# Performance work log

Hardware: AMD Instinct MI355X
Metric: run time of the kernel (lower is better)

The kernel has to match this reference:

```python
import jax, jax.numpy as jnp
import numpy as np

B, N, C = 2, 3072, 768
H = 12                      # num_heads
HD = C // H                 # 64
D = HD // 2                 # 32, rope dim per axis
GRID_H, GRID_W = 48, 64     # 768/16, 1024/16 ; GRID_H*GRID_W == N
BASE = 100.0
EPS = 1e-5


def _rope_tables():
    # positions per token (row-major cartesian product of y,x)
    pos_y = np.repeat(np.arange(GRID_H), GRID_W)   # [N]
    pos_x = np.tile(np.arange(GRID_W), GRID_H)     # [N]
    seq_len = max(GRID_H, GRID_W)
    inv_freq = 1.0 / BASE ** (np.arange(0, D, 2, dtype=np.float32) / D)  # [D/2]
    t = np.arange(seq_len, dtype=np.float32)
    freqs = np.einsum('i,j->ij', t, inv_freq)            # [S, D/2]
    emb = np.concatenate([freqs, freqs], axis=-1)        # [S, D]
    cos, sin = np.cos(emb), np.sin(emb)
    # gather per-token, add head broadcast dims -> [1, 1, N, D]
    mk = lambda tbl, idx: jnp.asarray(tbl[idx][None, None], dtype=jnp.float32)
    return mk(cos, pos_x), mk(sin, pos_x), mk(cos, pos_y), mk(sin, pos_y)


def setup_inputs() -> dict:
    key = jax.random.key(0)
    ks = jax.random.split(key, 12)
    s = 0.02
    cos_x, sin_x, cos_y, sin_y = _rope_tables()
    return {
        'x': jax.random.normal(ks[0], (B, N, C), jnp.float32),
        'w_qkv': jax.random.normal(ks[1], (3 * C, C), jnp.float32) * s,
        'w_proj': jax.random.normal(ks[2], (C, C), jnp.float32) * s,
        'b_proj': jnp.zeros((C,), jnp.float32),
        'g1': jnp.ones((C,), jnp.float32),
        'beta1': jnp.zeros((C,), jnp.float32),
        'g2': jnp.ones((C,), jnp.float32),
        'beta2': jnp.zeros((C,), jnp.float32),
        'w_fc1': jax.random.normal(ks[3], (4 * C, C), jnp.float32) * s,
        'b_fc1': jnp.zeros((4 * C,), jnp.float32),
        'w_fc2': jax.random.normal(ks[4], (C, 4 * C), jnp.float32) * s,
        'b_fc2': jnp.zeros((C,), jnp.float32),
        'cos_x': cos_x, 'sin_x': sin_x, 'cos_y': cos_y, 'sin_y': sin_y,
    }


def _layernorm(x, g, b):
    m = x.mean(-1, keepdims=True)
    v = ((x - m) ** 2).mean(-1, keepdims=True)
    return (x - m) * jax.lax.rsqrt(v + EPS) * g + b


def _rope1d(tok, cos, sin):
    t1, t2 = jnp.split(tok, 2, axis=-1)
    rot = jnp.concatenate([-t2, t1], axis=-1)
    return tok * cos + rot * sin


def _rope2d(tok, cos_x, sin_x, cos_y, sin_y):
    # tok: [B, H, N, HD]; first half of HD is y-coords, second half x-coords
    ty, tx = jnp.split(tok, 2, axis=-1)
    return jnp.concatenate([_rope1d(ty, cos_y, sin_y), _rope1d(tx, cos_x, sin_x)], axis=-1)


def reference(x, w_qkv, w_proj, b_proj, g1, beta1, g2, beta2,
              w_fc1, b_fc1, w_fc2, b_fc2, cos_x, sin_x, cos_y, sin_y):
    # --- attention branch ---
    xn = _layernorm(x, g1, beta1)
    qkv = jnp.einsum('bnc,dc->bnd', xn, w_qkv)           # [B, N, 3C]
    qkv = qkv.reshape(B, N, 3, H, HD).transpose(0, 3, 2, 1, 4)  # [B, H, 3, N, HD]
    q, k, v = qkv[:, :, 0], qkv[:, :, 1], qkv[:, :, 2]
    q = _rope2d(q, cos_x, sin_x, cos_y, sin_y)
    k = _rope2d(k, cos_x, sin_x, cos_y, sin_y)
    scale = HD ** -0.5
    attn = jnp.einsum('bhqd,bhkd->bhqk', q, k) * scale   # [B, H, N, N]
    attn = jax.nn.softmax(attn, axis=-1)
    o = jnp.einsum('bhqk,bhkd->bhqd', attn, v)           # [B, H, N, HD]
    o = o.transpose(0, 2, 1, 3).reshape(B, N, C)
    o = jnp.einsum('bnc,dc->bnd', o, w_proj) + b_proj
    x = x + o
    # --- mlp branch ---
    xn = _layernorm(x, g2, beta2)
    h = jnp.einsum('bnc,hc->bnh', xn, w_fc1) + b_fc1
    h = jax.nn.gelu(h, approximate=False)                # torch nn.GELU default (erf)
    h = jnp.einsum('bnh,ch->bnc', h, w_fc2) + b_fc2
    return x + h
```

## Files before the change

kernel.cpp:

```cpp
#include <hip/hip_runtime.h>
#include <hip/hip_bf16.h>


#define Nn 3072
#define Cc 768
#define Hh 12
#define Mm 6144

typedef unsigned short ushort_t;
typedef unsigned int u32;
using s8v = __attribute__((ext_vector_type(8))) short;
using f4v = __attribute__((ext_vector_type(4))) float;

__device__ __forceinline__ ushort_t f2b(float x){
  u32 u = __float_as_uint(x);
  return (ushort_t)((u + 0x7fffu + ((u >> 16) & 1u)) >> 16);
}
__device__ __forceinline__ u32 pack2(float a, float b){
  return (u32)f2b(a) | ((u32)f2b(b) << 16);
}
__device__ __forceinline__ u32 pack2t(float a, float b){
  return (__float_as_uint(a) >> 16) | (__float_as_uint(b) & 0xffff0000u);
}
__device__ __forceinline__ float b2f(ushort_t u){
  return __uint_as_float(((u32)u) << 16);
}

#define GLD16(g, l) __builtin_amdgcn_global_load_lds( \
    (const __attribute__((address_space(1))) u32*)(g), \
    (__attribute__((address_space(3))) u32*)(l), 16, 0, 0)

__global__ __launch_bounds__(256) void cvt4_kernel(
    const float* __restrict__ a, ushort_t* __restrict__ oa, int na,
    const float* __restrict__ b, ushort_t* __restrict__ ob, int nb,
    const float* __restrict__ c, ushort_t* __restrict__ oc, int nc,
    const float* __restrict__ d, ushort_t* __restrict__ od)
{
  int i = (blockIdx.x*256 + threadIdx.x)*4;
  const float* src; ushort_t* dst;
  if (i < na)           { src = a + i;            dst = oa + i; }
  else if (i < na+nb)   { src = b + (i-na);       dst = ob + (i-na); }
  else if (i < na+nb+nc){ src = c + (i-na-nb);    dst = oc + (i-na-nb); }
  else                  { src = d + (i-na-nb-nc); dst = od + (i-na-nb-nc); }
  float4 v = *(const float4*)src;
  uint2 p; p.x = pack2(v.x, v.y); p.y = pack2(v.z, v.w);
  *(uint2*)dst = p;
}

__global__ __launch_bounds__(256) void ln_kernel(const float* __restrict__ in,
    const float* __restrict__ g, const float* __restrict__ be, ushort_t* __restrict__ out)
{
  int row = blockIdx.x;
  int tid = threadIdx.x;
  size_t base = (size_t)row * Cc;
  float v[3];
  #pragma unroll
  for (int i = 0; i < 3; ++i) v[i] = in[base + tid + i*256];
  __shared__ float red[8];
  float s = v[0]+v[1]+v[2];
  #pragma unroll
  for (int off=32; off; off>>=1) s += __shfl_xor(s, off);
  int wid = tid >> 6, lane = tid & 63;
  if (lane==0) red[wid] = s;
  __syncthreads();
  float mean = (red[0]+red[1]+red[2]+red[3]) * (1.f/Cc);
  float d = 0.f;
  #pragma unroll
  for (int i=0;i<3;++i){ float t = v[i]-mean; d += t*t; }
  #pragma unroll
  for (int off=32; off; off>>=1) d += __shfl_xor(d, off);
  if (lane==0) red[4+wid] = d;
  __syncthreads();
  float var  = (red[4]+red[5]+red[6]+red[7]) * (1.f/Cc);
  float rstd = rsqrtf(var + 1e-5f);
  #pragma unroll
  for (int i=0;i<3;++i){
    int idx = tid + i*256;
    out[base+idx] = f2b((v[i]-mean)*rstd*g[idx] + be[idx]);
  }
}

template<int EPI>
__global__ __launch_bounds__(256) void mgemm_kernel(
    const ushort_t* __restrict__ A, const ushort_t* __restrict__ W,
    const float* __restrict__ bias, const float* __restrict__ residf,
    void* __restrict__ outv, int Nd, int K)
{
  __shared__ __align__(16) ushort_t As[128*32];
  __shared__ __align__(16) ushort_t Ws[128*32];
  int tid = threadIdx.x;
  int w = tid >> 6, lane = tid & 63;
  int g = lane >> 4, c = lane & 15;
  int wr = w >> 1, wc = w & 1;
  int m0 = blockIdx.y * 128, n0 = blockIdx.x * 128;
  int srow = w*32 + (lane >> 2);
  int schunk = (lane & 3) * 8;
  const ushort_t* Ag = A + (size_t)(m0 + srow)*K + schunk;
  const ushort_t* Wg = W + (size_t)(n0 + srow)*K + schunk;
  ushort_t* Asl = &As[w*1024];
  ushort_t* Wsl = &Ws[w*1024];
  f4v acc[4][4] = {};
  for (int k0 = 0; k0 < K; k0 += 32) {
    __syncthreads();
    GLD16(Ag + k0,        Asl);
    GLD16(Ag + 16*K + k0, Asl + 512);
    GLD16(Wg + k0,        Wsl);
    GLD16(Wg + 16*K + k0, Wsl + 512);
    __syncthreads();
    s8v af[4], wf[4];
    #pragma unroll
    for (int i=0;i<4;++i) af[i] = *(const s8v*)&As[(wr*64 + i*16 + c)*32 + g*8];
    #pragma unroll
    for (int j=0;j<4;++j) wf[j] = *(const s8v*)&Ws[(wc*64 + j*16 + c)*32 + g*8];
    #pragma unroll
    for (int i=0;i<4;++i)
      #pragma unroll
      for (int j=0;j<4;++j)
        acc[i][j] = __builtin_amdgcn_mfma_f32_16x16x32_bf16(af[i], wf[j], acc[i][j], 0,0,0);
  }
  #pragma unroll
  for (int j=0;j<4;++j){
    int col = n0 + wc*64 + j*16 + c;
    float bv = (EPI != 0) ? bias[col] : 0.f;
    #pragma unroll
    for (int i=0;i<4;++i){
      int row0 = m0 + wr*64 + i*16 + g*4;
      #pragma unroll
      for (int r=0;r<4;++r){
        float v = acc[i][j][r];
        size_t off = (size_t)(row0 + r)*Nd + col;
        if (EPI == 0) {
          ((ushort_t*)outv)[off] = f2b(v);
        } else if (EPI == 2) {
          float t = v + bv;
          ((ushort_t*)outv)[off] = f2b(0.5f*t*(1.0f + erff(t*0.70710678118654752f)));
        } else {
          ((float*)outv)[off] = v + bv + residf[off];
        }
      }
    }
  }
}

__global__ __launch_bounds__(256) void repack_kernel(
    const ushort_t* __restrict__ qkv,
    const float* __restrict__ cx, const float* __restrict__ sx,
    const float* __restrict__ cy, const float* __restrict__ sy,
    ushort_t* __restrict__ Qb, ushort_t* __restrict__ Kb, ushort_t* __restrict__ Vt)
{
  __shared__ float Vls[64*68];
  int bh = blockIdx.y;
  int b = bh / Hh, h = bh - b*Hh;
  int n0 = blockIdx.x * 64;
  int tid = threadIdx.x;
  int tt = tid >> 2, cch = tid & 3;
  int n = n0 + tt;
  size_t rowbase = (size_t)(b*Nn + n) * 2304 + h*64;

  int half = cch >> 1, ibase = (cch & 1) * 8;
  int d1 = half*32 + ibase;
  const float* ct  = half ? cx : cy;
  const float* st_ = half ? sx : sy;
  float c1[8], s1[8], c2[8], s2[8];
  #pragma unroll
  for (int j=0;j<8;++j){
    c1[j] = ct[n*32 + ibase + j];       s1[j] = st_[n*32 + ibase + j];
    c2[j] = ct[n*32 + ibase + 16 + j];  s2[j] = st_[n*32 + ibase + 16 + j];
  }
  #pragma unroll
  for (int qk = 0; qk < 2; ++qk){
    const ushort_t* src = qkv + rowbase + qk*768;
    uint4 uv1 = *(const uint4*)(src + d1);
    uint4 uv2 = *(const uint4*)(src + d1 + 16);
    float v1[8], v2[8];
    v1[0]=b2f(uv1.x&0xffff); v1[1]=b2f(uv1.x>>16); v1[2]=b2f(uv1.y&0xffff); v1[3]=b2f(uv1.y>>16);
    v1[4]=b2f(uv1.z&0xffff); v1[5]=b2f(uv1.z>>16); v1[6]=b2f(uv1.w&0xffff); v1[7]=b2f(uv1.w>>16);
    v2[0]=b2f(uv2.x&0xffff); v2[1]=b2f(uv2.x>>16); v2[2]=b2f(uv2.y&0xffff); v2[3]=b2f(uv2.y>>16);
    v2[4]=b2f(uv2.z&0xffff); v2[5]=b2f(uv2.z>>16); v2[6]=b2f(uv2.w&0xffff); v2[7]=b2f(uv2.w>>16);
    float sc = qk ? 1.0f : 0.125f;
    float o1[8], o2[8];
    #pragma unroll
    for (int j=0;j<8;++j){
      o1[j] = (v1[j]*c1[j] - v2[j]*s1[j]) * sc;
      o2[j] = (v2[j]*c2[j] + v1[j]*s2[j]) * sc;
    }
    ushort_t* dst = (qk ? Kb : Qb) + ((size_t)bh*Nn + n)*64;
    uint4 u1, u2;
    u1.x = pack2(o1[0],o1[1]); u1.y = pack2(o1[2],o1[3]);
    u1.z = pack2(o1[4],o1[5]); u1.w = pack2(o1[6],o1[7]);
    u2.x = pack2(o2[0],o2[1]); u2.y = pack2(o2[2],o2[3]);
    u2.z = pack2(o2[4],o2[5]); u2.w = pack2(o2[6],o2[7]);
    *(uint4*)(dst + d1)      = u1;
    *(uint4*)(dst + d1 + 16) = u2;
  }

  {
    const ushort_t* src = qkv + rowbase + 1536 + cch*16;
    uint4 ua = *(const uint4*)(src);
    uint4 ub = *(const uint4*)(src + 8);
    float* lp = &Vls[tt*68 + cch*16];
    lp[0]=b2f(ua.x&0xffff); lp[1]=b2f(ua.x>>16); lp[2]=b2f(ua.y&0xffff); lp[3]=b2f(ua.y>>16);
    lp[4]=b2f(ua.z&0xffff); lp[5]=b2f(ua.z>>16); lp[6]=b2f(ua.w&0xffff); lp[7]=b2f(ua.w>>16);
    lp[8]=b2f(ub.x&0xffff); lp[9]=b2f(ub.x>>16); lp[10]=b2f(ub.y&0xffff); lp[11]=b2f(ub.y>>16);
    lp[12]=b2f(ub.z&0xffff); lp[13]=b2f(ub.z>>16); lp[14]=b2f(ub.w&0xffff); lp[15]=b2f(ub.w>>16);
  }
  __syncthreads();
  {
    int d = tid & 63, quarter = tid >> 6;
    float v[16];
    #pragma unroll
    for (int j=0;j<16;++j) v[j] = Vls[(quarter*16 + j)*68 + d];
    uint4 w0, w1;
    w0.x = pack2(v[0],v[1]);   w0.y = pack2(v[2],v[3]);
    w0.z = pack2(v[4],v[5]);   w0.w = pack2(v[6],v[7]);
    w1.x = pack2(v[8],v[9]);   w1.y = pack2(v[10],v[11]);
    w1.z = pack2(v[12],v[13]); w1.w = pack2(v[14],v[15]);
    ushort_t* dst = Vt + ((size_t)bh*64 + d)*Nn + n0 + quarter*16;
    *(uint4*)(dst)     = w0;
    *(uint4*)(dst + 8) = w1;
  }
}

__global__ __launch_bounds__(256) void fattn_kernel(
    const ushort_t* __restrict__ Qb, const ushort_t* __restrict__ Kb,
    const ushort_t* __restrict__ Vt, ushort_t* __restrict__ ob)
{
  __shared__ ushort_t Ks[64*72];
  __shared__ ushort_t Vts[64*72];
  __shared__ ushort_t Ps[4*32*72];
  int bh = blockIdx.y;
  int q0 = blockIdx.x * 128;
  int tid = threadIdx.x;
  int w = tid >> 6, lane = tid & 63, g = lane >> 4, c = lane & 15;

  const ushort_t* qpA = Qb + ((size_t)bh*Nn + q0 + w*32 + c)*64;
  const ushort_t* qpB = qpA + 16*64;
  s8v qA0 = *(const s8v*)(qpA + g*8);
  s8v qA1 = *(const s8v*)(qpA + 32 + g*8);
  s8v qB0 = *(const s8v*)(qpB + g*8);
  s8v qB1 = *(const s8v*)(qpB + 32 + g*8);

  s8v ones8;
  #pragma unroll
  for (int j=0;j<8;++j) ones8[j] = (short)0x3f80;

  f4v oA[4] = {}, oB[4] = {}, lA = {0,0,0,0}, lB = {0,0,0,0};
  const ushort_t* kbase = Kb + (size_t)bh*Nn*64;
  const ushort_t* vbase = Vt + (size_t)bh*64*Nn;
  ushort_t* pwA = &Ps[w*32*72];
  ushort_t* pwB = pwA + 16*72;

  int srow = tid >> 2;
  int scb  = (tid & 3) * 16;

  for (int kt = 0; kt < Nn/64; ++kt){
    __syncthreads();
    {
      const ushort_t* ksrc = kbase + (size_t)(kt*64 + srow)*64 + scb;
      *(uint4*)&Ks[srow*72 + scb]     = *(const uint4*)(ksrc);
      *(uint4*)&Ks[srow*72 + scb + 8] = *(const uint4*)(ksrc + 8);
      const ushort_t* vsrc = vbase + (size_t)srow*Nn + kt*64 + scb;
      *(uint4*)&Vts[srow*72 + scb]     = *(const uint4*)(vsrc);
      *(uint4*)&Vts[srow*72 + scb + 8] = *(const uint4*)(vsrc + 8);
    }
    __syncthreads();

    f4v sA[4], sB[4];
    #pragma unroll
    for (int t=0;t<4;++t){
      s8v ka  = *(const s8v*)&Ks[(t*16+c)*72 + g*8];
      s8v kb2 = *(const s8v*)&Ks[(t*16+c)*72 + 32 + g*8];
      f4v z = {0,0,0,0};
      z = __builtin_amdgcn_mfma_f32_16x16x32_bf16(ka,  qA0, z, 0,0,0);
      sA[t] = __builtin_amdgcn_mfma_f32_16x16x32_bf16(kb2, qA1, z, 0,0,0);
      f4v z2 = {0,0,0,0};
      z2 = __builtin_amdgcn_mfma_f32_16x16x32_bf16(ka,  qB0, z2, 0,0,0);
      sB[t] = __builtin_amdgcn_mfma_f32_16x16x32_bf16(kb2, qB1, z2, 0,0,0);
    }
    #pragma unroll
    for (int t=0;t<4;++t){
      uint2 pk;
      pk.x = pack2t(__expf(sA[t][0]), __expf(sA[t][1]));
      pk.y = pack2t(__expf(sA[t][2]), __expf(sA[t][3]));
      *(uint2*)&pwA[c*72 + t*16 + g*4] = pk;
      pk.x = pack2t(__expf(sB[t][0]), __expf(sB[t][1]));
      pk.y = pack2t(__expf(sB[t][2]), __expf(sB[t][3]));
      *(uint2*)&pwB[c*72 + t*16 + g*4] = pk;
    }
    asm volatile("s_waitcnt lgkmcnt(0)" ::: "memory");
    s8v pA0 = *(const s8v*)&pwA[c*72 + g*8];
    s8v pA1 = *(const s8v*)&pwA[c*72 + 32 + g*8];
    s8v pB0 = *(const s8v*)&pwB[c*72 + g*8];
    s8v pB1 = *(const s8v*)&pwB[c*72 + 32 + g*8];

    #pragma unroll
    for (int d=0;d<4;++d){
      s8v va = *(const s8v*)&Vts[(d*16+c)*72 + g*8];
      s8v vb = *(const s8v*)&Vts[(d*16+c)*72 + 32 + g*8];
      oA[d] = __builtin_amdgcn_mfma_f32_16x16x32_bf16(va, pA0, oA[d], 0,0,0);
      oA[d] = __builtin_amdgcn_mfma_f32_16x16x32_bf16(vb, pA1, oA[d], 0,0,0);
      oB[d] = __builtin_amdgcn_mfma_f32_16x16x32_bf16(va, pB0, oB[d], 0,0,0);
      oB[d] = __builtin_amdgcn_mfma_f32_16x16x32_bf16(vb, pB1, oB[d], 0,0,0);
    }
    lA = __builtin_amdgcn_mfma_f32_16x16x32_bf16(ones8, pA0, lA, 0,0,0);
    lA = __builtin_amdgcn_mfma_f32_16x16x32_bf16(ones8, pA1, lA, 0,0,0);
    lB = __builtin_amdgcn_mfma_f32_16x16x32_bf16(ones8, pB0, lB, 0,0,0);
    lB = __builtin_amdgcn_mfma_f32_16x16x32_bf16(ones8, pB1, lB, 0,0,0);
  }

  int b = bh / Hh, h = bh - b*Hh;
  {
    float rl = 1.0f / lA[0];
    size_t tok = (size_t)b*Nn + q0 + w*32 + c;
    ushort_t* op = ob + tok*768 + h*64;
    #pragma unroll
    for (int d=0;d<4;++d){
      uint2 pk;
      pk.x = pack2(oA[d][0]*rl, oA[d][1]*rl);
      pk.y = pack2(oA[d][2]*rl, oA[d][3]*rl);
      *(uint2*)&op[d*16 + g*4] = pk;
    }
  }
  {
    float rl = 1.0f / lB[0];
    size_t tok = (size_t)b*Nn + q0 + w*32 + 16 + c;
    ushort_t* op = ob + tok*768 + h*64;
    #pragma unroll
    for (int d=0;d<4;++d){
      uint2 pk;
      pk.x = pack2(oB[d][0]*rl, oB[d][1]*rl);
      pk.y = pack2(oB[d][2]*rl, oB[d][3]*rl);
      *(uint2*)&op[d*16 + g*4] = pk;
    }
  }
}

extern "C" void kernel_launch(void* const* d_in, const int* in_sizes, int n_in,
                              void* d_out, int out_size, void* d_ws, size_t ws_size,
                              hipStream_t stream)
{
  const float* x      = (const float*)d_in[0];
  const float* w_qkv  = (const float*)d_in[1];
  const float* w_proj = (const float*)d_in[2];
  const float* b_proj = (const float*)d_in[3];
  const float* g1     = (const float*)d_in[4];
  const float* be1    = (const float*)d_in[5];
  const float* g2     = (const float*)d_in[6];
  const float* be2    = (const float*)d_in[7];
  const float* w_fc1  = (const float*)d_in[8];
  const float* b_fc1  = (const float*)d_in[9];
  const float* w_fc2  = (const float*)d_in[10];
  const float* b_fc2  = (const float*)d_in[11];
  const float* cx     = (const float*)d_in[12];
  const float* sx     = (const float*)d_in[13];
  const float* cy     = (const float*)d_in[14];
  const float* sy     = (const float*)d_in[15];
  float* out = (float*)d_out;

  char* ws = (char*)d_ws;
  ushort_t* xnb   = (ushort_t*)(ws);
  ushort_t* Qb    = (ushort_t*)(ws + 9437184);
  ushort_t* Kb    = (ushort_t*)(ws + 18874368);
  float*    x1    = (float*)   (ws + 9437184);
  ushort_t* Vt    = (ushort_t*)(ws + 28311552);
  ushort_t* obb   = (ushort_t*)(ws + 37748736);
  ushort_t* qkvb  = (ushort_t*)(ws + 47185920);
  ushort_t* hb    = (ushort_t*)(ws + 47185920);
  ushort_t* wqkvb = (ushort_t*)(ws + 84934656);
  ushort_t* wprojb= (ushort_t*)(ws + 88473600);
  ushort_t* wfc1b = (ushort_t*)(ws + 89653248);
  ushort_t* wfc2b = (ushort_t*)(ws + 94371840);

  cvt4_kernel<<<(7077888/4)/256, 256, 0, stream>>>(
      w_qkv, wqkvb, 2304*768, w_proj, wprojb, 768*768,
      w_fc1, wfc1b, 3072*768, w_fc2, wfc2b);

  ln_kernel<<<Mm, 256, 0, stream>>>(x, g1, be1, xnb);
  mgemm_kernel<0><<<dim3(2304/128, Mm/128), 256, 0, stream>>>(xnb, wqkvb, nullptr, nullptr, qkvb, 2304, 768);
  repack_kernel<<<dim3(48, 24), 256, 0, stream>>>(qkvb, cx, sx, cy, sy, Qb, Kb, Vt);
  fattn_kernel<<<dim3(24, 24), 256, 0, stream>>>(Qb, Kb, Vt, obb);
  mgemm_kernel<1><<<dim3(768/128, Mm/128), 256, 0, stream>>>(obb, wprojb, b_proj, x, x1, 768, 768);
  ln_kernel<<<Mm, 256, 0, stream>>>(x1, g2, be2, xnb);
  mgemm_kernel<2><<<dim3(3072/128, Mm/128), 256, 0, stream>>>(xnb, wfc1b, b_fc1, nullptr, hb, 3072, 768);
  mgemm_kernel<1><<<dim3(768/128, Mm/128), 256, 0, stream>>>(hb, wfc2b, b_fc2, x1, out, 768, 3072);
}
```

Before: 468.0 us.

## Split attention keys across waves and narrow GEMM tiles for N=768 projections

The attention kernel now processes 64 queries per block, and each of the four waves handles a disjoint quarter of the keys. Waves load K and V fragments straight from global memory instead of staging them through shared LDS with block barriers. Partial outputs and row sums are combined through LDS at the end, and the grid doubles to 48x24 blocks. The projection and fc2 GEMMs get a 64-wide N tile so they launch more blocks, at the cost of less reuse per tile and a bf16 rounding of the partial attention outputs before the reduction.

```diff
diff --git a/kernel.cpp b/kernel.cpp
--- a/kernel.cpp
+++ b/kernel.cpp
@@ -80,47 +80,49 @@
   }
 }
 
-template<int EPI>
+template<int EPI, int NT>
 __global__ __launch_bounds__(256) void mgemm_kernel(
     const ushort_t* __restrict__ A, const ushort_t* __restrict__ W,
     const float* __restrict__ bias, const float* __restrict__ residf,
     void* __restrict__ outv, int Nd, int K)
 {
+  constexpr int JT = NT/32;
   __shared__ __align__(16) ushort_t As[128*32];
-  __shared__ __align__(16) ushort_t Ws[128*32];
+  __shared__ __align__(16) ushort_t Ws[NT*32];
   int tid = threadIdx.x;
   int w = tid >> 6, lane = tid & 63;
   int g = lane >> 4, c = lane & 15;
   int wr = w >> 1, wc = w & 1;
-  int m0 = blockIdx.y * 128, n0 = blockIdx.x * 128;
-  int srow = w*32 + (lane >> 2);
+  int m0 = blockIdx.y * 128, n0 = blockIdx.x * NT;
   int schunk = (lane & 3) * 8;
-  const ushort_t* Ag = A + (size_t)(m0 + srow)*K + schunk;
-  const ushort_t* Wg = W + (size_t)(n0 + srow)*K + schunk;
+  const ushort_t* Ag = A + (size_t)(m0 + w*32 + (lane >> 2))*K + schunk;
+  const ushort_t* Wg;
+  if constexpr (NT == 128) Wg = W + (size_t)(n0 + w*32 + (lane >> 2))*K + schunk;
+  else                     Wg = W + (size_t)(n0 + w*16 + (lane >> 2))*K + schunk;
   ushort_t* Asl = &As[w*1024];
-  ushort_t* Wsl = &Ws[w*1024];
-  f4v acc[4][4] = {};
+  ushort_t* Wsl = (NT == 128) ? &Ws[w*1024] : &Ws[w*512];
+  f4v acc[4][JT] = {};
   for (int k0 = 0; k0 < K; k0 += 32) {
     __syncthreads();
     GLD16(Ag + k0,        Asl);
     GLD16(Ag + 16*K + k0, Asl + 512);
     GLD16(Wg + k0,        Wsl);
-    GLD16(Wg + 16*K + k0, Wsl + 512);
+    if constexpr (NT == 128) GLD16(Wg + 16*K + k0, Wsl + 512);
     __syncthreads();
-    s8v af[4], wf[4];
+    s8v af[4], wf[JT];
     #pragma unroll
     for (int i=0;i<4;++i) af[i] = *(const s8v*)&As[(wr*64 + i*16 + c)*32 + g*8];
     #pragma unroll
-    for (int j=0;j<4;++j) wf[j] = *(const s8v*)&Ws[(wc*64 + j*16 + c)*32 + g*8];
+    for (int j=0;j<JT;++j) wf[j] = *(const s8v*)&Ws[(wc*(NT/2) + j*16 + c)*32 + g*8];
     #pragma unroll
     for (int i=0;i<4;++i)
       #pragma unroll
-      for (int j=0;j<4;++j)
+      for (int j=0;j<JT;++j)
         acc[i][j] = __builtin_amdgcn_mfma_f32_16x16x32_bf16(af[i], wf[j], acc[i][j], 0,0,0);
   }
   #pragma unroll
-  for (int j=0;j<4;++j){
-    int col = n0 + wc*64 + j*16 + c;
+  for (int j=0;j<JT;++j){
+    int col = n0 + wc*(NT/2) + j*16 + c;
     float bv = (EPI != 0) ? bias[col] : 0.f;
     #pragma unroll
     for (int i=0;i<4;++i){
@@ -221,118 +223,117 @@
   }
 }
 
-__global__ __launch_bounds__(256) void fattn_kernel(
+__global__ __launch_bounds__(256, 2) void fattn_kernel(
     const ushort_t* __restrict__ Qb, const ushort_t* __restrict__ Kb,
     const ushort_t* __restrict__ Vt, ushort_t* __restrict__ ob)
 {
-  __shared__ ushort_t Ks[64*72];
-  __shared__ ushort_t Vts[64*72];
-  __shared__ ushort_t Ps[4*32*72];
+  __shared__ __align__(16) char smem[36864];
+  __shared__ float Lred[256];
   int bh = blockIdx.y;
-  int q0 = blockIdx.x * 128;
+  int q0 = blockIdx.x * 64;
   int tid = threadIdx.x;
   int w = tid >> 6, lane = tid & 63, g = lane >> 4, c = lane & 15;
 
-  const ushort_t* qpA = Qb + ((size_t)bh*Nn + q0 + w*32 + c)*64;
-  const ushort_t* qpB = qpA + 16*64;
-  s8v qA0 = *(const s8v*)(qpA + g*8);
-  s8v qA1 = *(const s8v*)(qpA + 32 + g*8);
-  s8v qB0 = *(const s8v*)(qpB + g*8);
-  s8v qB1 = *(const s8v*)(qpB + 32 + g*8);
-
-  s8v ones8;
-  #pragma unroll
-  for (int j=0;j<8;++j) ones8[j] = (short)0x3f80;
-
-  f4v oA[4] = {}, oB[4] = {}, lA = {0,0,0,0}, lB = {0,0,0,0};
   const ushort_t* kbase = Kb + (size_t)bh*Nn*64;
   const ushort_t* vbase = Vt + (size_t)bh*64*Nn;
-  ushort_t* pwA = &Ps[w*32*72];
-  ushort_t* pwB = pwA + 16*72;
-
-  int srow = tid >> 2;
-  int scb  = (tid & 3) * 16;
-
-  for (int kt = 0; kt < Nn/64; ++kt){
-    __syncthreads();
-    {
-      const ushort_t* ksrc = kbase + (size_t)(kt*64 + srow)*64 + scb;
-      *(uint4*)&Ks[srow*72 + scb]     = *(const uint4*)(ksrc);
-      *(uint4*)&Ks[srow*72 + scb + 8] = *(const uint4*)(ksrc + 8);
-      const ushort_t* vsrc = vbase + (size_t)srow*Nn + kt*64 + scb;
-      *(uint4*)&Vts[srow*72 + scb]     = *(const uint4*)(vsrc);
-      *(uint4*)&Vts[srow*72 + scb + 8] = *(const uint4*)(vsrc + 8);
-    }
-    __syncthreads();
-
-    f4v sA[4], sB[4];
-    #pragma unroll
-    for (int t=0;t<4;++t){
-      s8v ka  = *(const s8v*)&Ks[(t*16+c)*72 + g*8];
-      s8v kb2 = *(const s8v*)&Ks[(t*16+c)*72 + 32 + g*8];
-      f4v z = {0,0,0,0};
-      z = __builtin_amdgcn_mfma_f32_16x16x32_bf16(ka,  qA0, z, 0,0,0);
-      sA[t] = __builtin_amdgcn_mfma_f32_16x16x32_bf16(kb2, qA1, z, 0,0,0);
-      f4v z2 = {0,0,0,0};
-      z2 = __builtin_amdgcn_mfma_f32_16x16x32_bf16(ka,  qB0, z2, 0,0,0);
-      sB[t] = __builtin_amdgcn_mfma_f32_16x16x32_bf16(kb2, qB1, z2, 0,0,0);
-    }
-    #pragma unroll
-    for (int t=0;t<4;++t){
-      uint2 pk;
-      pk.x = pack2t(__expf(sA[t][0]), __expf(sA[t][1]));
-      pk.y = pack2t(__expf(sA[t][2]), __expf(sA[t][3]));
-      *(uint2*)&pwA[c*72 + t*16 + g*4] = pk;
-      pk.x = pack2t(__expf(sB[t][0]), __expf(sB[t][1]));
-      pk.y = pack2t(__expf(sB[t][2]), __expf(sB[t][3]));
-      *(uint2*)&pwB[c*72 + t*16 + g*4] = pk;
+
+  s8v qf0[4], qf1[4];
+  #pragma unroll
+  for (int qs=0;qs<4;++qs){
+    const ushort_t* qp = Qb + ((size_t)bh*Nn + q0 + qs*16 + c)*64;
+    qf0[qs] = *(const s8v*)(qp + g*8);
+    qf1[qs] = *(const s8v*)(qp + 32 + g*8);
+  }
+  s8v ones8;
+  #pragma unroll
+  for (int j=0;j<8;++j) ones8[j] = (short)0x3f80;
+
+  f4v o[4][4] = {};
+  f4v l[4] = {};
+  ushort_t* pw = (ushort_t*)smem + w*4608;
+
+  for (int it = 0; it < 12; ++it){
+    int key0 = (it*4 + w) * 64;
+    s8v ka[4], kb2[4];
+    #pragma unroll
+    for (int ks=0;ks<4;++ks){
+      const ushort_t* kr = kbase + (size_t)(key0 + ks*16 + c)*64 + g*8;
+      ka[ks]  = *(const s8v*)(kr);
+      kb2[ks] = *(const s8v*)(kr + 32);
+    }
+    #pragma unroll
+    for (int qs=0;qs<4;++qs){
+      #pragma unroll
+      for (int ks=0;ks<4;++ks){
+        f4v z = {0,0,0,0};
+        z = __builtin_amdgcn_mfma_f32_16x16x32_bf16(ka[ks],  qf0[qs], z, 0,0,0);
+        z = __builtin_amdgcn_mfma_f32_16x16x32_bf16(kb2[ks], qf1[qs], z, 0,0,0);
+        uint2 pk;
+        pk.x = pack2t(__expf(z[0]), __expf(z[1]));
+        pk.y = pack2t(__expf(z[2]), __expf(z[3]));
+        *(uint2*)&pw[qs*1152 + c*72 + ks*16 + g*4] = pk;
+      }
     }
     asm volatile("s_waitcnt lgkmcnt(0)" ::: "memory");
-    s8v pA0 = *(const s8v*)&pwA[c*72 + g*8];
-    s8v pA1 = *(const s8v*)&pwA[c*72 + 32 + g*8];
-    s8v pB0 = *(const s8v*)&pwB[c*72 + g*8];
-    s8v pB1 = *(const s8v*)&pwB[c*72 + 32 + g*8];
-
+    s8v va[4], vb[4];
     #pragma unroll
     for (int d=0;d<4;++d){
-      s8v va = *(const s8v*)&Vts[(d*16+c)*72 + g*8];
-      s8v vb = *(const s8v*)&Vts[(d*16+c)*72 + 32 + g*8];
-      oA[d] = __builtin_amdgcn_mfma_f32_16x16x32_bf16(va, pA0, oA[d], 0,0,0);
-      oA[d] = __builtin_amdgcn_mfma_f32_16x16x32_bf16(vb, pA1, oA[d], 0,0,0);
-      oB[d] = __builtin_amdgcn_mfma_f32_16x16x32_bf16(va, pB0, oB[d], 0,0,0);
-      oB[d] = __builtin_amdgcn_mfma_f32_16x16x32_bf16(vb, pB1, oB[d], 0,0,0);
-    }
-    lA = __builtin_amdgcn_mfma_f32_16x16x32_bf16(ones8, pA0, lA, 0,0,0);
-    lA = __builtin_amdgcn_mfma_f32_16x16x32_bf16(ones8, pA1, lA, 0,0,0);
-    lB = __builtin_amdgcn_mfma_f32_16x16x32_bf16(ones8, pB0, lB, 0,0,0);
-    lB = __builtin_amdgcn_mfma_f32_16x16x32_bf16(ones8, pB1, lB, 0,0,0);
-  }
-
-  int b = bh / Hh, h = bh - b*Hh;
-  {
-    float rl = 1.0f / lA[0];
-    size_t tok = (size_t)b*Nn + q0 + w*32 + c;
-    ushort_t* op = ob + tok*768 + h*64;
+      const ushort_t* vr = vbase + (size_t)(d*16 + c)*Nn + key0 + g*8;
+      va[d] = *(const s8v*)(vr);
+      vb[d] = *(const s8v*)(vr + 32);
+    }
+    #pragma unroll
+    for (int qs=0;qs<4;++qs){
+      s8v pf0 = *(const s8v*)&pw[qs*1152 + c*72 + g*8];
+      s8v pf1 = *(const s8v*)&pw[qs*1152 + c*72 + 32 + g*8];
+      #pragma unroll
+      for (int d=0;d<4;++d){
+        o[qs][d] = __builtin_amdgcn_mfma_f32_16x16x32_bf16(va[d], pf0, o[qs][d], 0,0,0);
+        o[qs][d] = __builtin_amdgcn_mfma_f32_16x16x32_bf16(vb[d], pf1, o[qs][d], 0,0,0);
+      }
+      l[qs] = __builtin_amdgcn_mfma_f32_16x16x32_bf16(ones8, pf0, l[qs], 0,0,0);
+      l[qs] = __builtin_amdgcn_mfma_f32_16x16x32_bf16(ones8, pf1, l[qs], 0,0,0);
+    }
+  }
+
+  ushort_t* Or = (ushort_t*)smem;
+  #pragma unroll
+  for (int qs=0;qs<4;++qs){
     #pragma unroll
     for (int d=0;d<4;++d){
       uint2 pk;
-      pk.x = pack2(oA[d][0]*rl, oA[d][1]*rl);
-      pk.y = pack2(oA[d][2]*rl, oA[d][3]*rl);
-      *(uint2*)&op[d*16 + g*4] = pk;
-    }
-  }
-  {
-    float rl = 1.0f / lB[0];
-    size_t tok = (size_t)b*Nn + q0 + w*32 + 16 + c;
-    ushort_t* op = ob + tok*768 + h*64;
-    #pragma unroll
-    for (int d=0;d<4;++d){
-      uint2 pk;
-      pk.x = pack2(oB[d][0]*rl, oB[d][1]*rl);
-      pk.y = pack2(oB[d][2]*rl, oB[d][3]*rl);
-      *(uint2*)&op[d*16 + g*4] = pk;
-    }
-  }
+      pk.x = pack2(o[qs][d][0], o[qs][d][1]);
+      pk.y = pack2(o[qs][d][2], o[qs][d][3]);
+      *(uint2*)&Or[(w*64 + qs*16 + c)*72 + d*16 + g*4] = pk;
+    }
+    Lred[w*64 + qs*16 + c] = l[qs][0];
+  }
+  __syncthreads();
+
+  int qrow = tid >> 2, dseg = (tid & 3) * 16;
+  float acc[16] = {};
+  #pragma unroll
+  for (int w2=0;w2<4;++w2){
+    const ushort_t* base = &Or[(w2*64 + qrow)*72 + dseg];
+    uint4 u0 = *(const uint4*)(base);
+    uint4 u1 = *(const uint4*)(base + 8);
+    u32 uu[8] = {u0.x,u0.y,u0.z,u0.w,u1.x,u1.y,u1.z,u1.w};
+    #pragma unroll
+    for (int j=0;j<8;++j){
+      acc[j*2]   += b2f((ushort_t)(uu[j] & 0xffff));
+      acc[j*2+1] += b2f((ushort_t)(uu[j] >> 16));
+    }
+  }
+  float rl = 1.0f / (Lred[qrow] + Lred[64+qrow] + Lred[128+qrow] + Lred[192+qrow]);
+  int b = bh / Hh, h = bh - b*Hh;
+  ushort_t* op = ob + ((size_t)b*Nn + q0 + qrow)*768 + h*64 + dseg;
+  uint4 w0_, w1_;
+  w0_.x = pack2(acc[0]*rl, acc[1]*rl);   w0_.y = pack2(acc[2]*rl, acc[3]*rl);
+  w0_.z = pack2(acc[4]*rl, acc[5]*rl);   w0_.w = pack2(acc[6]*rl, acc[7]*rl);
+  w1_.x = pack2(acc[8]*rl, acc[9]*rl);   w1_.y = pack2(acc[10]*rl, acc[11]*rl);
+  w1_.z = pack2(acc[12]*rl, acc[13]*rl); w1_.w = pack2(acc[14]*rl, acc[15]*rl);
+  *(uint4*)(op)     = w0_;
+  *(uint4*)(op + 8) = w1_;
 }
 
 extern "C" void kernel_launch(void* const* d_in, const int* in_sizes, int n_in,
@@ -376,11 +377,11 @@
       w_fc1, wfc1b, 3072*768, w_fc2, wfc2b);
 
   ln_kernel<<<Mm, 256, 0, stream>>>(x, g1, be1, xnb);
-  mgemm_kernel<0><<<dim3(2304/128, Mm/128), 256, 0, stream>>>(xnb, wqkvb, nullptr, nullptr, qkvb, 2304, 768);
+  mgemm_kernel<0,128><<<dim3(2304/128, Mm/128), 256, 0, stream>>>(xnb, wqkvb, nullptr, nullptr, qkvb, 2304, 768);
   repack_kernel<<<dim3(48, 24), 256, 0, stream>>>(qkvb, cx, sx, cy, sy, Qb, Kb, Vt);
-  fattn_kernel<<<dim3(24, 24), 256, 0, stream>>>(Qb, Kb, Vt, obb);
-  mgemm_kernel<1><<<dim3(768/128, Mm/128), 256, 0, stream>>>(obb, wprojb, b_proj, x, x1, 768, 768);
+  fattn_kernel<<<dim3(48, 24), 256, 0, stream>>>(Qb, Kb, Vt, obb);
+  mgemm_kernel<1,64><<<dim3(768/64, Mm/128), 256, 0, stream>>>(obb, wprojb, b_proj, x, x1, 768, 768);
   ln_kernel<<<Mm, 256, 0, stream>>>(x1, g2, be2, xnb);
-  mgemm_kernel<2><<<dim3(3072/128, Mm/128), 256, 0, stream>>>(xnb, wfc1b, b_fc1, nullptr, hb, 3072, 768);
-  mgemm_kernel<1><<<dim3(768/128, Mm/128), 256, 0, stream>>>(hb, wfc2b, b_fc2, x1, out, 768, 3072);
-}
+  mgemm_kernel<2,128><<<dim3(3072/128, Mm/128), 256, 0, stream>>>(xnb, wfc1b, b_fc1, nullptr, hb, 3072, 768);
+  mgemm_kernel<1,64><<<dim3(768/64, Mm/128), 256, 0, stream>>>(hb, wfc2b, b_fc2, x1, out, 768, 3072);
+}
```

Result: faster. 458.1 us (-2.1%).
